# Optimization experiments

Hardware: AMD Instinct MI355X
Metric: run time of the kernel (lower is better)

Reference implementation:

```python
import jax, jax.numpy as jnp
import numpy as np

B, T, C, H = 4, 2048, 1024, 16
HD = C // H  # head_dim = 64


def setup_inputs() -> dict:
    key = jax.random.key(0)
    k1, k2, k3, k4, k5 = jax.random.split(key, 5)
    s = 1.0 / np.sqrt(C)
    return {
        "x": jax.random.normal(k1, (B, T, C), dtype=jnp.float32),
        "Wqkv": jax.random.normal(k2, (C, 3 * C), dtype=jnp.float32) * s,
        "bqkv": jnp.zeros((3 * C,), dtype=jnp.float32),
        "Wproj": jax.random.normal(k3, (C, C), dtype=jnp.float32) * s,
        "bproj": jnp.zeros((C,), dtype=jnp.float32),
    }


def reference(x, Wqkv, bqkv, Wproj, bproj):
    b, t, c = x.shape
    qkv = x @ Wqkv + bqkv                      # [B,T,3C]
    q, k, v = jnp.split(qkv, 3, axis=-1)
    # [B,T,C] -> [B,H,T,HD]
    q = q.reshape(b, t, H, HD).transpose(0, 2, 1, 3)
    k = k.reshape(b, t, H, HD).transpose(0, 2, 1, 3)
    v = v.reshape(b, t, H, HD).transpose(0, 2, 1, 3)
    att = jnp.einsum("bhqd,bhkd->bhqk", q, k) * (1.0 / np.sqrt(HD))
    causal = jnp.tril(jnp.ones((t, t), dtype=bool))
    att = jnp.where(causal[None, None], att, -jnp.inf)
    att = jax.nn.softmax(att, axis=-1)
    # dropout p=0.0 (eval) -> identity
    y = jnp.einsum("bhqk,bhkd->bhqd", att, v)  # [B,H,T,HD]
    y = y.transpose(0, 2, 1, 3).reshape(b, t, c)
    return y @ Wproj + bproj
```

## Files before the change

### kernel.cpp

```cpp
#include <hip/hip_runtime.h>


typedef unsigned short u16;
typedef short short8_t __attribute__((ext_vector_type(8)));
typedef float f32x4 __attribute__((ext_vector_type(4)));

#define B_ 4
#define T_ 2048
#define C_ 1024
#define H_ 16
#define HD_ 64
#define QSCALE 0.18033688011112042f

__device__ __forceinline__ u16 f32_to_bf16(float f) {
  unsigned int u = __float_as_uint(f);
  u += 0x7fffu + ((u >> 16) & 1u);
  return (u16)(u >> 16);
}

__device__ __forceinline__ void async_copy16(const void* g, void* l) {
  __builtin_amdgcn_global_load_lds((const __attribute__((address_space(1))) void*)g,
                                   (__attribute__((address_space(3))) void*)l, 16, 0, 0);
}

__global__ void cast_x_kernel(const float* __restrict__ in, u16* __restrict__ out) {
  int i = blockIdx.x * 256 + threadIdx.x;
  float4 v = ((const float4*)in)[i];
  unsigned int a = (unsigned int)f32_to_bf16(v.x) | ((unsigned int)f32_to_bf16(v.y) << 16);
  unsigned int b = (unsigned int)f32_to_bf16(v.z) | ((unsigned int)f32_to_bf16(v.w) << 16);
  ((uint2*)out)[i] = make_uint2(a, b);
}

__global__ void transpose_cast_kernel(const float* __restrict__ in, u16* __restrict__ out,
                                      int K, int N) {
  __shared__ float tile[32][33];
  int nb = blockIdx.x * 32, kb = blockIdx.y * 32;
  int c = threadIdx.x & 31, r0 = threadIdx.x >> 5;
#pragma unroll
  for (int rr = 0; rr < 4; ++rr) {
    int r = r0 + rr * 8;
    tile[r][c] = in[(size_t)(kb + r) * N + nb + c];
  }
  __syncthreads();
#pragma unroll
  for (int rr = 0; rr < 4; ++rr) {
    int r = r0 + rr * 8;
    out[(size_t)(nb + r) * K + kb + c] = f32_to_bf16(tile[c][r]);
  }
}

__device__ __forceinline__ void stage_tile(const u16* __restrict__ A, const u16* __restrict__ Bt,
                                           int K, int m0, int n0, int k0, char* buf, int tid) {
#pragma unroll
  for (int it = 0; it < 2; ++it) {
    int j = it * 256 + tid;
    int row = j >> 2;
    int ch = ((j & 3) ^ (row >> 1)) & 3;
    async_copy16(A + (size_t)(m0 + row) * K + k0 + ch * 8, buf + j * 16);
    async_copy16(Bt + (size_t)(n0 + row) * K + k0 + ch * 8, buf + 8192 + j * 16);
  }
}

__device__ __forceinline__ void gemm_mainloop(const u16* __restrict__ A, const u16* __restrict__ Bt,
                                              int K, int m0, int n0, char* smem,
                                              f32x4 (&acc)[4][4]) {
  int tid = threadIdx.x;
  int lane = tid & 63, wave = tid >> 6;
  int quad = lane >> 4, l15 = lane & 15;
  int waveM = wave >> 1, waveN = wave & 1;
  stage_tile(A, Bt, K, m0, n0, 0, smem, tid);
  int nIter = K >> 5;
  for (int ki = 0; ki < nIter; ++ki) {
    int cur = ki & 1;
    char* bufc = smem + cur * 16384;
    __syncthreads();
    if (ki + 1 < nIter)
      stage_tile(A, Bt, K, m0, n0, (ki + 1) << 5, smem + (cur ^ 1) * 16384, tid);
    short8_t af[4], bfr[4];
#pragma unroll
    for (int mt = 0; mt < 4; ++mt) {
      int row = waveM * 64 + mt * 16 + l15;
      af[mt] = *(const short8_t*)(bufc + row * 64 + (((quad ^ (row >> 1)) & 3) << 4));
    }
#pragma unroll
    for (int nt = 0; nt < 4; ++nt) {
      int row = waveN * 64 + nt * 16 + l15;
      bfr[nt] = *(const short8_t*)(bufc + 8192 + row * 64 + (((quad ^ (row >> 1)) & 3) << 4));
    }
#pragma unroll
    for (int mt = 0; mt < 4; ++mt)
#pragma unroll
      for (int nt = 0; nt < 4; ++nt)
        acc[mt][nt] = __builtin_amdgcn_mfma_f32_16x16x32_bf16(af[mt], bfr[nt], acc[mt][nt], 0, 0, 0);
  }
}

__global__ __launch_bounds__(256, 2) void gemm1_kernel(const u16* __restrict__ A,
                                                       const u16* __restrict__ Bt,
                                                       const float* __restrict__ bias,
                                                       u16* __restrict__ Qo, u16* __restrict__ Ko,
                                                       u16* __restrict__ Vo) {
  __shared__ __align__(128) char smem[32768];
  f32x4 acc[4][4];
#pragma unroll
  for (int mt = 0; mt < 4; ++mt)
#pragma unroll
    for (int nt = 0; nt < 4; ++nt) acc[mt][nt] = (f32x4){0.f, 0.f, 0.f, 0.f};
  int m0 = blockIdx.y * 128, n0 = blockIdx.x * 128;
  gemm_mainloop(A, Bt, C_, m0, n0, smem, acc);

  int lane = threadIdx.x & 63, wave = threadIdx.x >> 6;
  int quad = lane >> 4, l15 = lane & 15;
  int waveM = wave >> 1, waveN = wave & 1;

  if (n0 < 2048) {
#pragma unroll
    for (int nt = 0; nt < 4; ++nt) {
      int n = n0 + waveN * 64 + nt * 16;
      int which = n >> 10;
      int rem = n & 1023;
      int head = rem >> 6;
      int d = (rem & 63) + l15;
      float bv = bias[n + l15];
      float sc = (which == 0) ? QSCALE : 1.0f;
      u16* dst = (which == 0) ? Qo : Ko;
#pragma unroll
      for (int mt = 0; mt < 4; ++mt) {
#pragma unroll
        for (int r = 0; r < 4; ++r) {
          int token = m0 + waveM * 64 + mt * 16 + quad * 4 + r;
          int b = token >> 11, t = token & 2047;
          dst[(((size_t)(b * H_ + head)) * T_ + t) * HD_ + d] =
              f32_to_bf16((acc[mt][nt][r] + bv) * sc);
        }
      }
    }
  } else {
    __syncthreads();
    char* W = smem + wave * 8192;
#pragma unroll
    for (int nt = 0; nt < 4; ++nt) {
      int nl = nt * 16 + l15;
      float bv = bias[n0 + waveN * 64 + nl];
#pragma unroll
      for (int mt = 0; mt < 4; ++mt) {
        int g = mt * 4 + quad;
        int pc = ((g >> 1) ^ (nl & 7)) & 7;
        uint2 pv;
        pv.x = (unsigned int)f32_to_bf16(acc[mt][nt][0] + bv) |
               ((unsigned int)f32_to_bf16(acc[mt][nt][1] + bv) << 16);
        pv.y = (unsigned int)f32_to_bf16(acc[mt][nt][2] + bv) |
               ((unsigned int)f32_to_bf16(acc[mt][nt][3] + bv) << 16);
        *(uint2*)(W + nl * 128 + pc * 16 + (g & 1) * 8) = pv;
      }
    }
    int b = m0 >> 11;
#pragma unroll
    for (int i = 0; i < 8; ++i) {
      int jj = i * 64 + lane;
      int nl = jj >> 3;
      int c = jj & 7;
      int pc = c ^ (nl & 7);
      uint4 v = *(const uint4*)(W + nl * 128 + pc * 16);
      int rem = (n0 - 2048) + waveN * 64 + nl;
      int head = rem >> 6, dd = rem & 63;
      int t0 = (m0 & 2047) + waveM * 64 + c * 8;
      *(uint4*)(Vo + ((size_t)(b * H_ + head) * HD_ + dd) * T_ + t0) = v;
    }
  }
}

__global__ __launch_bounds__(256, 2) void gemm2_kernel(const u16* __restrict__ A,
                                                       const u16* __restrict__ Bt,
                                                       const float* __restrict__ bias,
                                                       float* __restrict__ out) {
  __shared__ __align__(128) char smem[32768];
  f32x4 acc[4][4];
#pragma unroll
  for (int mt = 0; mt < 4; ++mt)
#pragma unroll
    for (int nt = 0; nt < 4; ++nt) acc[mt][nt] = (f32x4){0.f, 0.f, 0.f, 0.f};
  int m0 = blockIdx.y * 128, n0 = blockIdx.x * 128;
  gemm_mainloop(A, Bt, C_, m0, n0, smem, acc);

  int lane = threadIdx.x & 63, wave = threadIdx.x >> 6;
  int quad = lane >> 4, l15 = lane & 15;
  int waveM = wave >> 1, waveN = wave & 1;
#pragma unroll
  for (int nt = 0; nt < 4; ++nt) {
    int col = n0 + waveN * 64 + nt * 16 + l15;
    float bv = bias[col];
#pragma unroll
    for (int mt = 0; mt < 4; ++mt) {
#pragma unroll
      for (int r = 0; r < 4; ++r) {
        int token = m0 + waveM * 64 + mt * 16 + quad * 4 + r;
        out[(size_t)token * C_ + col] = acc[mt][nt][r] + bv;
      }
    }
  }
}

__device__ __forceinline__ void stage_kv(const u16* __restrict__ Kb, const u16* __restrict__ Vb,
                                         int kt, char* Ksb, char* Vsb, int tid) {
#pragma unroll
  for (int it = 0; it < 2; ++it) {
    int j = it * 256 + tid;
    int row = j >> 3;
    int ch = (j & 7) ^ (row & 7);
    async_copy16(Kb + (size_t)(kt * 64 + row) * HD_ + ch * 8, Ksb + j * 16);
    async_copy16(Vb + (size_t)row * T_ + kt * 64 + ch * 8, Vsb + j * 16);
  }
}

__global__ __launch_bounds__(256, 3) void attn_kernel(const u16* __restrict__ Qg,
                                                      const u16* __restrict__ Kg,
                                                      const u16* __restrict__ Vg,
                                                      u16* __restrict__ Yg) {
  __shared__ __align__(128) char smem[49152];
  int tid = threadIdx.x;
  int wave = tid >> 6, lane = tid & 63;
  int quad = lane >> 4, l15 = lane & 15;
  char* Psw = smem + 32768 + wave * 4096;
  int bh = blockIdx.x;
  int qt = 15 - blockIdx.y;
  int b = bh >> 4, h = bh & 15;
  const u16* Kb = Kg + (size_t)bh * T_ * HD_;
  const u16* Vb = Vg + (size_t)bh * HD_ * T_;

  short8_t qf[2][2];
#pragma unroll
  for (int mt = 0; mt < 2; ++mt)
#pragma unroll
    for (int ks = 0; ks < 2; ++ks) {
      int row = qt * 128 + wave * 32 + mt * 16 + l15;
      qf[mt][ks] = *(const short8_t*)(Qg + ((size_t)bh * T_ + row) * HD_ + ks * 32 + quad * 8);
    }

  stage_kv(Kb, Vb, 0, smem, smem + 16384, tid);

  float l_part[2][4];
  f32x4 o[2][4];
#pragma unroll
  for (int mt = 0; mt < 2; ++mt)
#pragma unroll
    for (int r = 0; r < 4; ++r) l_part[mt][r] = 0.f;
#pragma unroll
  for (int mt = 0; mt < 2; ++mt)
#pragma unroll
    for (int dt = 0; dt < 4; ++dt) o[mt][dt] = (f32x4){0.f, 0.f, 0.f, 0.f};

  int ktmax_blk = 2 * qt + 1;
  int ktmax_wave = 2 * qt + (wave >> 1);
  for (int kt = 0; kt <= ktmax_blk; ++kt) {
    int cur = kt & 1;
    char* Ksc = smem + cur * 8192;
    char* Vtc = smem + 16384 + cur * 8192;
    __syncthreads();
    if (kt < ktmax_blk)
      stage_kv(Kb, Vb, kt + 1, smem + (cur ^ 1) * 8192, smem + 16384 + (cur ^ 1) * 8192, tid);
    if (kt > ktmax_wave) continue;

    f32x4 s[2][4];
#pragma unroll
    for (int mt = 0; mt < 2; ++mt)
#pragma unroll
      for (int nt = 0; nt < 4; ++nt) s[mt][nt] = (f32x4){0.f, 0.f, 0.f, 0.f};
#pragma unroll
    for (int ks = 0; ks < 2; ++ks) {
      short8_t bfr[4];
#pragma unroll
      for (int nt = 0; nt < 4; ++nt) {
        int row = nt * 16 + l15;
        bfr[nt] = *(const short8_t*)(Ksc + row * 128 + ((((ks * 4 + quad) ^ row) & 7) << 4));
      }
#pragma unroll
      for (int mt = 0; mt < 2; ++mt)
#pragma unroll
        for (int nt = 0; nt < 4; ++nt)
          s[mt][nt] =
              __builtin_amdgcn_mfma_f32_16x16x32_bf16(qf[mt][ks], bfr[nt], s[mt][nt], 0, 0, 0);
    }

    if (kt == ktmax_wave) {
#pragma unroll
      for (int mt = 0; mt < 2; ++mt) {
        int qrow0 = qt * 128 + wave * 32 + mt * 16 + quad * 4;
#pragma unroll
        for (int nt = 0; nt < 4; ++nt) {
          int col = kt * 64 + nt * 16 + l15;
#pragma unroll
          for (int r = 0; r < 4; ++r) {
            float p = __builtin_amdgcn_exp2f(s[mt][nt][r]);
            if (col > qrow0 + r) p = 0.f;
            s[mt][nt][r] = p;
          }
        }
      }
    } else {
#pragma unroll
      for (int mt = 0; mt < 2; ++mt)
#pragma unroll
        for (int nt = 0; nt < 4; ++nt)
#pragma unroll
          for (int r = 0; r < 4; ++r) s[mt][nt][r] = __builtin_amdgcn_exp2f(s[mt][nt][r]);
    }

#pragma unroll
    for (int mt = 0; mt < 2; ++mt) {
#pragma unroll
      for (int r = 0; r < 4; ++r)
        l_part[mt][r] += (s[mt][0][r] + s[mt][1][r]) + (s[mt][2][r] + s[mt][3][r]);
#pragma unroll
      for (int nt = 0; nt < 4; ++nt) {
        int col = nt * 16 + l15;
#pragma unroll
        for (int r = 0; r < 4; ++r) {
          int prow = mt * 16 + quad * 4 + r;
          *(u16*)(Psw + prow * 128 + ((((col >> 3) ^ prow) & 7) << 4) + ((col & 7) << 1)) =
              (u16)(__float_as_uint(s[mt][nt][r]) >> 16);
        }
      }
    }

#pragma unroll
    for (int ks = 0; ks < 2; ++ks) {
      short8_t af[2], bfr[4];
#pragma unroll
      for (int mt = 0; mt < 2; ++mt) {
        int row = mt * 16 + l15;
        af[mt] = *(const short8_t*)(Psw + row * 128 + ((((ks * 4 + quad) ^ row) & 7) << 4));
      }
#pragma unroll
      for (int dt = 0; dt < 4; ++dt) {
        int row = dt * 16 + l15;
        bfr[dt] = *(const short8_t*)(Vtc + row * 128 + ((((ks * 4 + quad) ^ row) & 7) << 4));
      }
#pragma unroll
      for (int mt = 0; mt < 2; ++mt)
#pragma unroll
        for (int dt = 0; dt < 4; ++dt)
          o[mt][dt] = __builtin_amdgcn_mfma_f32_16x16x32_bf16(af[mt], bfr[dt], o[mt][dt], 0, 0, 0);
    }
  }

#pragma unroll
  for (int mt = 0; mt < 2; ++mt) {
#pragma unroll
    for (int r = 0; r < 4; ++r) {
      float lsum = l_part[mt][r];
#pragma unroll
      for (int off = 1; off < 16; off <<= 1) lsum += __shfl_xor(lsum, off);
      float inv = 1.0f / lsum;
#pragma unroll
      for (int dt = 0; dt < 4; ++dt) {
        int t = qt * 128 + wave * 32 + mt * 16 + quad * 4 + r;
        float val = o[mt][dt][r] * inv;
        Yg[((size_t)(b * T_ + t)) * C_ + h * HD_ + dt * 16 + l15] = f32_to_bf16(val);
      }
    }
  }
}

extern "C" void kernel_launch(void* const* d_in, const int* in_sizes, int n_in,
                              void* d_out, int out_size, void* d_ws, size_t ws_size,
                              hipStream_t stream) {
  (void)in_sizes; (void)n_in; (void)out_size; (void)ws_size;
  const float* x = (const float*)d_in[0];
  const float* Wqkv = (const float*)d_in[1];
  const float* bqkv = (const float*)d_in[2];
  const float* Wproj = (const float*)d_in[3];
  const float* bproj = (const float*)d_in[4];
  float* out = (float*)d_out;
  char* ws = (char*)d_ws;

  u16* Xb = (u16*)ws;
  u16* WqkvT = (u16*)(ws + 16777216);
  u16* WprojT = (u16*)(ws + 16777216 + 6291456);
  u16* Q = (u16*)(ws + 25165824);
  u16* K = Q + 8388608;
  u16* V = K + 8388608;
  u16* Y = Xb;

  cast_x_kernel<<<8192, 256, 0, stream>>>(x, Xb);
  transpose_cast_kernel<<<dim3(96, 32), 256, 0, stream>>>(Wqkv, WqkvT, C_, 3 * C_);
  transpose_cast_kernel<<<dim3(32, 32), 256, 0, stream>>>(Wproj, WprojT, C_, C_);
  gemm1_kernel<<<dim3(24, 64), 256, 0, stream>>>(Xb, WqkvT, bqkv, Q, K, V);
  attn_kernel<<<dim3(64, 16), 256, 0, stream>>>(Q, K, V, Y);
  gemm2_kernel<<<dim3(8, 64), 256, 0, stream>>>(Y, WprojT, bproj, out);
}
```

Measured before the change: 238.9 us.

## Swizzle GEMM block order, shrink proj GEMM tile, prioritize MFMA waves

```diff
diff --git a/kernel.cpp b/kernel.cpp
--- a/kernel.cpp
+++ b/kernel.cpp
@@ -106,7 +106,10 @@
   for (int mt = 0; mt < 4; ++mt)
 #pragma unroll
     for (int nt = 0; nt < 4; ++nt) acc[mt][nt] = (f32x4){0.f, 0.f, 0.f, 0.f};
-  int m0 = blockIdx.y * 128, n0 = blockIdx.x * 128;
+  int flat = blockIdx.y * 24 + blockIdx.x;
+  int swz = (flat & 7) * 192 + (flat >> 3);
+  int n0 = (swz % 24) * 128;
+  int m0 = (swz / 24) * 128;
   gemm_mainloop(A, Bt, C_, m0, n0, smem, acc);
 
   int lane = threadIdx.x & 63, wave = threadIdx.x >> 6;
@@ -170,25 +173,73 @@
   }
 }
 
-__global__ __launch_bounds__(256, 2) void gemm2_kernel(const u16* __restrict__ A,
+__device__ __forceinline__ void stage_tile_g2(const u16* __restrict__ A,
+                                              const u16* __restrict__ Bt, int m0, int n0, int k0,
+                                              char* buf, int tid) {
+#pragma unroll
+  for (int it = 0; it < 2; ++it) {
+    int j = it * 256 + tid;
+    int row = j >> 2;
+    int ch = ((j & 3) ^ (row >> 1)) & 3;
+    async_copy16(A + (size_t)(m0 + row) * C_ + k0 + ch * 8, buf + j * 16);
+  }
+  {
+    int j = tid;
+    int row = j >> 2;
+    int ch = ((j & 3) ^ (row >> 1)) & 3;
+    async_copy16(Bt + (size_t)(n0 + row) * C_ + k0 + ch * 8, buf + 8192 + j * 16);
+  }
+}
+
+__global__ __launch_bounds__(256, 4) void gemm2_kernel(const u16* __restrict__ A,
                                                        const u16* __restrict__ Bt,
                                                        const float* __restrict__ bias,
                                                        float* __restrict__ out) {
-  __shared__ __align__(128) char smem[32768];
-  f32x4 acc[4][4];
+  __shared__ __align__(128) char smem[24576];
+  f32x4 acc[4][2];
 #pragma unroll
   for (int mt = 0; mt < 4; ++mt)
 #pragma unroll
-    for (int nt = 0; nt < 4; ++nt) acc[mt][nt] = (f32x4){0.f, 0.f, 0.f, 0.f};
-  int m0 = blockIdx.y * 128, n0 = blockIdx.x * 128;
-  gemm_mainloop(A, Bt, C_, m0, n0, smem, acc);
-
-  int lane = threadIdx.x & 63, wave = threadIdx.x >> 6;
+    for (int nt = 0; nt < 2; ++nt) acc[mt][nt] = (f32x4){0.f, 0.f, 0.f, 0.f};
+  int flat = blockIdx.y * 16 + blockIdx.x;
+  int swz = (flat & 7) * 128 + (flat >> 3);
+  int n0 = (swz & 15) * 64;
+  int m0 = (swz >> 4) * 128;
+
+  int tid = threadIdx.x;
+  int lane = tid & 63, wave = tid >> 6;
   int quad = lane >> 4, l15 = lane & 15;
   int waveM = wave >> 1, waveN = wave & 1;
-#pragma unroll
-  for (int nt = 0; nt < 4; ++nt) {
-    int col = n0 + waveN * 64 + nt * 16 + l15;
+
+  stage_tile_g2(A, Bt, m0, n0, 0, smem, tid);
+  int nIter = C_ >> 5;
+  for (int ki = 0; ki < nIter; ++ki) {
+    int cur = ki & 1;
+    char* bufc = smem + cur * 12288;
+    __syncthreads();
+    if (ki + 1 < nIter)
+      stage_tile_g2(A, Bt, m0, n0, (ki + 1) << 5, smem + (cur ^ 1) * 12288, tid);
+    short8_t af[4], bfr[2];
+#pragma unroll
+    for (int mt = 0; mt < 4; ++mt) {
+      int row = waveM * 64 + mt * 16 + l15;
+      af[mt] = *(const short8_t*)(bufc + row * 64 + (((quad ^ (row >> 1)) & 3) << 4));
+    }
+#pragma unroll
+    for (int nt = 0; nt < 2; ++nt) {
+      int row = waveN * 32 + nt * 16 + l15;
+      bfr[nt] = *(const short8_t*)(bufc + 8192 + row * 64 + (((quad ^ (row >> 1)) & 3) << 4));
+    }
+#pragma unroll
+    for (int mt = 0; mt < 4; ++mt)
+#pragma unroll
+      for (int nt = 0; nt < 2; ++nt)
+        acc[mt][nt] = __builtin_amdgcn_mfma_f32_16x16x32_bf16(af[mt], bfr[nt], acc[mt][nt], 0, 0, 0);
+  }
+
+#pragma unroll
+  for (int nt = 0; nt < 2; ++nt) {
+    int col = n0 + waveN * 32 + nt * 16 + l15;
     float bv = bias[col];
 #pragma unroll
     for (int mt = 0; mt < 4; ++mt) {
@@ -274,12 +325,14 @@
         int row = nt * 16 + l15;
         bfr[nt] = *(const short8_t*)(Ksc + row * 128 + ((((ks * 4 + quad) ^ row) & 7) << 4));
       }
+      __builtin_amdgcn_s_setprio(1);
 #pragma unroll
       for (int mt = 0; mt < 2; ++mt)
 #pragma unroll
         for (int nt = 0; nt < 4; ++nt)
           s[mt][nt] =
               __builtin_amdgcn_mfma_f32_16x16x32_bf16(qf[mt][ks], bfr[nt], s[mt][nt], 0, 0, 0);
+      __builtin_amdgcn_s_setprio(0);
     }
 
     if (kt == ktmax_wave) {
@@ -336,11 +389,13 @@
         int row = dt * 16 + l15;
         bfr[dt] = *(const short8_t*)(Vtc + row * 128 + ((((ks * 4 + quad) ^ row) & 7) << 4));
       }
+      __builtin_amdgcn_s_setprio(1);
 #pragma unroll
       for (int mt = 0; mt < 2; ++mt)
 #pragma unroll
         for (int dt = 0; dt < 4; ++dt)
           o[mt][dt] = __builtin_amdgcn_mfma_f32_16x16x32_bf16(af[mt], bfr[dt], o[mt][dt], 0, 0, 0);
+      __builtin_amdgcn_s_setprio(0);
     }
   }
 
@@ -387,5 +442,5 @@
   transpose_cast_kernel<<<dim3(32, 32), 256, 0, stream>>>(Wproj, WprojT, C_, C_);
   gemm1_kernel<<<dim3(24, 64), 256, 0, stream>>>(Xb, WqkvT, bqkv, Q, K, V);
   attn_kernel<<<dim3(64, 16), 256, 0, stream>>>(Q, K, V, Y);
-  gemm2_kernel<<<dim3(8, 64), 256, 0, stream>>>(Y, WprojT, bproj, out);
-}
+  gemm2_kernel<<<dim3(16, 64), 256, 0, stream>>>(Y, WprojT, bproj, out);
+}
```

Measured after the change: 246.9 us. +3.3%, slower.
